# Optimization experiments

Measured on AMD Instinct MI355X. Metric: run time of the kernel, lower is better.

## Reference

```python
import jax, jax.numpy as jnp
import numpy as np

B, L, D, H = 2, 2048, 1024, 16
HD = D // H  # head_dim = 64


def setup_inputs() -> dict:
    key = jax.random.key(0)
    ks = jax.random.split(key, 11)
    s = 1.0 / np.sqrt(D)
    return {
        "query": jax.random.normal(ks[0], (B, L, D), jnp.float32),
        "key_": jax.random.normal(ks[1], (B, L, D), jnp.float32),
        "value": jax.random.normal(ks[2], (B, L, D), jnp.float32),
        "Wq": jax.random.normal(ks[3], (D, D), jnp.float32) * s,
        "bq": jnp.zeros((D,), jnp.float32),
        "Wk": jax.random.normal(ks[4], (D, D), jnp.float32) * s,
        "bk": jnp.zeros((D,), jnp.float32),
        "Wv": jax.random.normal(ks[5], (D, D), jnp.float32) * s,
        "bv": jnp.zeros((D,), jnp.float32),
        "Wo": jax.random.normal(ks[6], (D, D), jnp.float32) * s,
        "bo": jnp.zeros((D,), jnp.float32),
    }


def reference(query, key_, value, Wq, bq, Wk, bk, Wv, bv, Wo, bo):
    # q/k/v projections -> [B, H, L, HD]
    q = (query @ Wq + bq).reshape(B, L, H, HD).transpose(0, 2, 1, 3)
    k = (key_ @ Wk + bk).reshape(B, L, H, HD).transpose(0, 2, 1, 3)
    v = (value @ Wv + bv).reshape(B, L, H, HD).transpose(0, 2, 1, 3)
    # full attention matrix [B, H, L, L], scaled by sqrt(head_dim)
    scores = jnp.einsum('bhqd,bhkd->bhqk', q, k) / jnp.sqrt(jnp.float32(HD))
    attn = jax.nn.softmax(scores, axis=-1)
    out = jnp.einsum('bhqk,bhkd->bhqd', attn, v)  # [B, H, L, HD]
    out = out.transpose(0, 2, 1, 3).reshape(B, L, D)
    return out @ Wo + bo
```

## Files before the change

kernel.cpp:

```cpp
#include <hip/hip_runtime.h>
#include <hip/hip_bf16.h>
#include <stdint.h>

#define BATCH   2
#define SEQ     2048
#define D_MODEL 1024
#define NHEADS  16
#define HEADDIM 64
#define M_ROWS  (BATCH * SEQ)
#define NSPLIT  2

typedef __attribute__((ext_vector_type(8))) short bf16x8;
typedef __attribute__((ext_vector_type(4))) float f32x4;
typedef __attribute__((ext_vector_type(16))) float f32x16;
typedef __attribute__((ext_vector_type(2))) unsigned uint2v;

typedef __attribute__((address_space(3))) void       lds_void;
typedef const __attribute__((address_space(1))) void glb_void;

#define GLD_LDS16(g, l) \
  __builtin_amdgcn_global_load_lds((glb_void*)(g), (lds_void*)(l), 16, 0, 0)

#if __has_builtin(__builtin_amdgcn_exp2f)
#define EXP2(x) __builtin_amdgcn_exp2f(x)
#else
#define EXP2(x) exp2f(x)
#endif

__device__ __forceinline__ unsigned short f2bf(float f) {
  union { float f; unsigned u; } v; v.f = f;
  unsigned r = v.u + 0x7fff + ((v.u >> 16) & 1);
  return (unsigned short)(r >> 16);
}

__device__ __forceinline__ float bf2f(unsigned short u) {
  union { unsigned u; float f; } v; v.u = ((unsigned)u) << 16; return v.f;
}

__device__ __forceinline__ unsigned pkbf(float a, float b) {
  __hip_bfloat162 h = __float22bfloat162_rn(float2{a, b});
  union { __hip_bfloat162 h; unsigned u; } cv; cv.h = h; return cv.u;
}

__device__ __forceinline__ void plane32_swap(unsigned& a, unsigned& b) {
#if __has_builtin(__builtin_amdgcn_permlane32_swap)
  uint2v r = __builtin_amdgcn_permlane32_swap(a, b, false, false);
  a = r[0]; b = r[1];
#else
  asm volatile("s_nop 1\n\tv_permlane32_swap_b32 %0, %1\n\ts_nop 1"
               : "+v"(a), "+v"(b));
#endif
}

struct Cvt3Args { const float* x[3]; unsigned short* y[3]; };
__global__ void cvt_bf16_3(Cvt3Args a, int n) {
  const float* x = a.x[blockIdx.z];
  unsigned short* y = a.y[blockIdx.z];
  int i = (blockIdx.x * blockDim.x + threadIdx.x) * 4;
  if (i + 3 < n) {
    float4 v = *(const float4*)(x + i);
    ushort4 o; o.x = f2bf(v.x); o.y = f2bf(v.y); o.z = f2bf(v.z); o.w = f2bf(v.w);
    *(ushort4*)(y + i) = o;
  }
}

struct Wt4Args { const float* W[4]; unsigned short* WT[4]; };
__global__ void wtrans4(Wt4Args a) {
  const float* W = a.W[blockIdx.z];
  unsigned short* WT = a.WT[blockIdx.z];
  __shared__ float t[32][33];
  int bx = blockIdx.x * 32, by = blockIdx.y * 32;
  int tx = threadIdx.x, ty = threadIdx.y;
  t[ty][tx] = W[(size_t)(by + ty) * D_MODEL + bx + tx];
  __syncthreads();
  WT[(size_t)(bx + ty) * D_MODEL + by + tx] = f2bf(t[tx][ty]);
}

struct GemmArgs {
  const unsigned short* A[3];
  const unsigned short* B[3];
  const float*          bias[3];
  void*                 dst[3];
  int                   mode0;
};

__global__ __launch_bounds__(512, 2) void gemm_bf16(GemmArgs ga) {
  const int L = blockIdx.x;
  const int xcd = L & 7, slot = L >> 3;
  const int cb   = slot & 7;
  const int rest = slot >> 3;
  const int pp   = rest & 3;
  const int z    = rest >> 2;
  const int panel = pp * 8 + xcd;
  const int bn0 = cb * 128, bm0 = panel * 128;

  const unsigned short* __restrict__ A  = ga.A[z];
  const unsigned short* __restrict__ BT = ga.B[z];
  const float* __restrict__ bias        = ga.bias[z];
  void* dst = ga.dst[z];
  const int mode = ga.mode0 + z;

  const int K = D_MODEL;
  __shared__ unsigned short lds_a[128 * 64];
  __shared__ unsigned short lds_b[128 * 64];
  const int tid = threadIdx.x, wave = tid >> 6, lane = tid & 63;
  const int wr = wave >> 2, wc = wave & 3;
  const int lr = lane & 15, lq = lane >> 4;
  const int r8 = lane >> 3;
  const int sc = (lane & 7) ^ r8;

  f32x4 acc[4][2] = {};

  for (int k0 = 0; k0 < K; k0 += 64) {
    __syncthreads();
#pragma unroll
    for (int it = 0; it < 2; ++it) {
      int row = it * 64 + wave * 8 + r8;
      GLD_LDS16(A  + (size_t)(bm0 + row) * K + k0 + sc * 8,
                lds_a + (it * 512 + wave * 64) * 8);
      GLD_LDS16(BT + (size_t)(bn0 + row) * K + k0 + sc * 8,
                lds_b + (it * 512 + wave * 64) * 8);
    }
    __syncthreads();

#pragma unroll
    for (int kk = 0; kk < 2; ++kk) {
      bf16x8 af[4], bfr[2];
#pragma unroll
      for (int i = 0; i < 4; ++i) {
        const int ra = wr * 64 + i * 16 + lr;
        af[i] = *(const bf16x8*)(lds_a + ra * 64 + (((kk * 4 + lq) ^ (lr & 7)) * 8));
      }
#pragma unroll
      for (int j = 0; j < 2; ++j) {
        const int rb = wc * 32 + j * 16 + lr;
        bfr[j] = *(const bf16x8*)(lds_b + rb * 64 + (((kk * 4 + lq) ^ (lr & 7)) * 8));
      }
#pragma unroll
      for (int mi = 0; mi < 4; ++mi)
#pragma unroll
        for (int ni = 0; ni < 2; ++ni)
          acc[mi][ni] = __builtin_amdgcn_mfma_f32_16x16x32_bf16(af[mi], bfr[ni], acc[mi][ni], 0, 0, 0);
    }
  }

#pragma unroll
  for (int mi = 0; mi < 4; ++mi) {
#pragma unroll
    for (int ni = 0; ni < 2; ++ni) {
      const int n  = bn0 + wc * 32 + ni * 16 + lr;
      const float bv = bias[n];
      const int mb = bm0 + wr * 64 + mi * 16 + lq * 4;
      f32x4 v = acc[mi][ni];
      if (mode == 3) {
        float* o = (float*)dst;
#pragma unroll
        for (int r = 0; r < 4; ++r) o[(size_t)(mb + r) * D_MODEL + n] = v[r] + bv;
      } else if (mode == 2) {
        const int b = mb >> 11, l = mb & 2047;
        const int h = n >> 6, hd = n & 63;
        ushort4 pk;
        pk.x = f2bf(v[0] + bv); pk.y = f2bf(v[1] + bv);
        pk.z = f2bf(v[2] + bv); pk.w = f2bf(v[3] + bv);
        *(ushort4*)((unsigned short*)dst + ((size_t)((b * NHEADS + h) * HEADDIM + hd)) * SEQ + l) = pk;
      } else {
        unsigned short* o = (unsigned short*)dst;
        const int h = n >> 6, hd = n & 63;
#pragma unroll
        for (int r = 0; r < 4; ++r) {
          int m = mb + r; int b = m >> 11, l = m & 2047;
          o[((size_t)(b * NHEADS + h) * SEQ + l) * HEADDIM + hd] = f2bf(v[r] + bv);
        }
      }
    }
  }
}

__global__ __launch_bounds__(512, 4) void flash_attn(
    const unsigned short* __restrict__ Q,
    const unsigned short* __restrict__ Kb,
    const unsigned short* __restrict__ VT,
    unsigned short* __restrict__ Opart,
    float* __restrict__ lsum) {
  const int L = blockIdx.x;
  const int xcd = L & 7, slot = L >> 3;
  const int head = xcd * 4 + (slot >> 4);
  const int split = (slot >> 3) & 1;
  const int qb   = slot & 7;
  const int b = head >> 4, h = head & 15;
  const int kbase = split * (SEQ / NSPLIT);

  const int tid = threadIdx.x, wave = tid >> 6, lane = tid & 63;
  const int l31 = lane & 31, hi = lane >> 5;
  const int q0 = qb * 256 + wave * 32;

  const unsigned short* Qh = Q  + (size_t)head * SEQ * HEADDIM;
  const unsigned short* Kh = Kb + (size_t)head * SEQ * HEADDIM;
  const unsigned short* Vh = VT + (size_t)head * HEADDIM * SEQ;

  __shared__ unsigned short ldsK[2][64 * 64];
  __shared__ unsigned short ldsV[2][64 * 64];

  const int r8 = lane >> 3;
  const int sc = (lane & 7) ^ r8;
#define STAGE_KV(buf, k0_)                                                          \
  {                                                                                 \
    int row = wave * 8 + r8;                                                        \
    GLD_LDS16(Kh + (size_t)(k0_ + row) * HEADDIM + sc * 8,                          \
              &ldsK[buf][wave * 512]);                                              \
    GLD_LDS16(Vh + (size_t)row * SEQ + (k0_) + sc * 8,                              \
              &ldsV[buf][wave * 512]);                                              \
  }

  bf16x8 qf[4];
#pragma unroll
  for (int ds = 0; ds < 4; ++ds)
    qf[ds] = *(const bf16x8*)(Qh + (size_t)(q0 + l31) * HEADDIM + ds * 16 + hi * 8);

  f32x16 oacc[2] = {};
  float lpA = 0.f, lpB = 0.f;
  const float C  = 0.18033688011112f;
  const float nm = -C * 8.0f;

  STAGE_KV(0, kbase);
  __syncthreads();
  int cur = 0;

  const int NT = SEQ / NSPLIT / 64;
  for (int t = 0; t < NT; ++t) {
    if (t + 1 < NT) STAGE_KV(cur ^ 1, kbase + (t + 1) * 64);

    const unsigned short* lk = ldsK[cur];
    const unsigned short* lv = ldsV[cur];

    unsigned u[2][8];
#pragma unroll
    for (int kt = 0; kt < 2; ++kt) {
      const int row = kt * 32 + l31;
      const int swz = row & 7;
      f32x16 s = {};
      __builtin_amdgcn_s_setprio(1);
#pragma unroll
      for (int ds = 0; ds < 4; ++ds) {
        bf16x8 kf = *(const bf16x8*)(lk + row * 64 + (((ds * 2 + hi) ^ swz) * 8));
        s = __builtin_amdgcn_mfma_f32_32x32x16_bf16(kf, qf[ds], s, 0, 0, 0);
      }
      __builtin_amdgcn_s_setprio(0);
#pragma unroll
      for (int m = 0; m < 8; ++m) {
        float p0 = EXP2(fmaf(s[2 * m],     C, nm));
        float p1 = EXP2(fmaf(s[2 * m + 1], C, nm));
        lpA += p0; lpB += p1;
        u[kt][m] = pkbf(p0, p1);
      }
    }

    __builtin_amdgcn_s_setprio(1);
#pragma unroll
    for (int ks = 0; ks < 4; ++ks) {
      const int kt = ks >> 1, a = 4 * (ks & 1);
      unsigned c0 = u[kt][a],     c2 = u[kt][a + 2];
      unsigned c1 = u[kt][a + 1], c3 = u[kt][a + 3];
      plane32_swap(c0, c2);
      plane32_swap(c1, c3);
      union { unsigned w[4]; bf16x8 v; } pf;
      pf.w[0] = c0; pf.w[1] = c1; pf.w[2] = c2; pf.w[3] = c3;
#pragma unroll
      for (int dt = 0; dt < 2; ++dt) {
        const int row = dt * 32 + l31;
        bf16x8 vf = *(const bf16x8*)(lv + row * 64 + (((ks * 2 + hi) ^ (row & 7)) * 8));
        oacc[dt] = __builtin_amdgcn_mfma_f32_32x32x16_bf16(pf.v, vf, oacc[dt], 0, 0, 0);
      }
    }
    __builtin_amdgcn_s_setprio(0);

    __syncthreads();
    cur ^= 1;
  }

  float lpart = lpA + lpB;
  lpart += __shfl_xor(lpart, 32);
  float iv = 1.f / lpart;
  unsigned short* Opw = Opart + (size_t)split * M_ROWS * D_MODEL;
#pragma unroll
  for (int reg = 0; reg < 16; ++reg) {
    int qrow = (reg & 3) + 8 * (reg >> 2) + 4 * hi;
    float ivr = __shfl(iv, qrow);
    int qi = q0 + qrow;
#pragma unroll
    for (int dt = 0; dt < 2; ++dt)
      Opw[((size_t)(b * SEQ + qi) * NHEADS + h) * HEADDIM + dt * 32 + l31] =
          f2bf(oacc[dt][reg] * ivr);
  }
  if (hi == 0)
    lsum[((size_t)split * 32 + head) * SEQ + q0 + l31] = lpart;
#undef STAGE_KV
}

__global__ void combine2(const unsigned short* __restrict__ Op,
                         const float* __restrict__ lsum,
                         unsigned short* __restrict__ Obuf) {
  size_t i8 = ((size_t)blockIdx.x * blockDim.x + threadIdx.x) * 8;
  int row = (int)(i8 >> 10), col = (int)(i8 & 1023);
  int b = row >> 11, q = row & 2047;
  int head = b * NHEADS + (col >> 6);
  float l1 = lsum[(size_t)head * SEQ + q];
  float l2 = lsum[(size_t)(32 + head) * SEQ + q];
  float inv = 1.f / (l1 + l2);
  float w1 = l1 * inv, w2 = l2 * inv;
  bf16x8 a = *(const bf16x8*)(Op + i8);
  bf16x8 c = *(const bf16x8*)(Op + (size_t)M_ROWS * D_MODEL + i8);
  union { unsigned short u[8]; bf16x8 v; } o;
#pragma unroll
  for (int j = 0; j < 8; ++j)
    o.u[j] = f2bf(w1 * bf2f((unsigned short)a[j]) + w2 * bf2f((unsigned short)c[j]));
  *(bf16x8*)(Obuf + i8) = o.v;
}

extern "C" void kernel_launch(void* const* d_in, const int* in_sizes, int n_in,
                              void* d_out, int out_size, void* d_ws, size_t ws_size,
                              hipStream_t stream) {
  const float* query = (const float*)d_in[0];
  const float* key_  = (const float*)d_in[1];
  const float* value = (const float*)d_in[2];
  const float* Wq = (const float*)d_in[3];
  const float* bq = (const float*)d_in[4];
  const float* Wk = (const float*)d_in[5];
  const float* bk = (const float*)d_in[6];
  const float* Wv = (const float*)d_in[7];
  const float* bv = (const float*)d_in[8];
  const float* Wo = (const float*)d_in[9];
  const float* bo = (const float*)d_in[10];

  const size_t NX = (size_t)M_ROWS * D_MODEL;
  const size_t NW = (size_t)D_MODEL * D_MODEL;

  char* ws = (char*)d_ws;
  size_t off = 0;
  auto alloc = [&](size_t bytes) { char* p = ws + off; off += (bytes + 255) & ~255ULL; return p; };
  unsigned short* Xq    = (unsigned short*)alloc(NX * 2);
  unsigned short* Xk    = (unsigned short*)alloc(NX * 2);
  unsigned short* Xv    = (unsigned short*)alloc(NX * 2);
  unsigned short* WqT   = (unsigned short*)alloc(NW * 2);
  unsigned short* WkT   = (unsigned short*)alloc(NW * 2);
  unsigned short* WvT   = (unsigned short*)alloc(NW * 2);
  unsigned short* WoT   = (unsigned short*)alloc(NW * 2);
  unsigned short* Qh    = (unsigned short*)alloc(NX * 2);
  unsigned short* Kh    = (unsigned short*)alloc(NX * 2);
  unsigned short* VTh   = (unsigned short*)alloc(NX * 2);
  unsigned short* Obuf  = (unsigned short*)alloc(NX * 2);
  unsigned short* Opart = (unsigned short*)alloc(NSPLIT * NX * 2);
  float*          lbuf  = (float*)alloc(NSPLIT * 32 * SEQ * sizeof(float));

  Cvt3Args ca;
  ca.x[0] = query; ca.x[1] = key_; ca.x[2] = value;
  ca.y[0] = Xq;    ca.y[1] = Xk;   ca.y[2] = Xv;
  cvt_bf16_3<<<dim3((unsigned)(NX / 4 / 256), 1, 3), 256, 0, stream>>>(ca, (int)NX);

  Wt4Args wa;
  wa.W[0] = Wq; wa.W[1] = Wk; wa.W[2] = Wv; wa.W[3] = Wo;
  wa.WT[0] = WqT; wa.WT[1] = WkT; wa.WT[2] = WvT; wa.WT[3] = WoT;
  wtrans4<<<dim3(32, 32, 4), dim3(32, 32), 0, stream>>>(wa);

  GemmArgs pa = {};
  pa.A[0] = Xq;  pa.A[1] = Xk;  pa.A[2] = Xv;
  pa.B[0] = WqT; pa.B[1] = WkT; pa.B[2] = WvT;
  pa.bias[0] = bq; pa.bias[1] = bk; pa.bias[2] = bv;
  pa.dst[0] = Qh; pa.dst[1] = Kh; pa.dst[2] = VTh;
  pa.mode0 = 0;
  gemm_bf16<<<768, 512, 0, stream>>>(pa);

  flash_attn<<<512, 512, 0, stream>>>(Qh, Kh, VTh, Opart, lbuf);

  combine2<<<(unsigned)(NX / 8 / 256), 256, 0, stream>>>(Opart, lbuf, Obuf);

  GemmArgs fa = {};
  fa.A[0] = Obuf; fa.B[0] = WoT; fa.bias[0] = bo; fa.dst[0] = d_out; fa.mode0 = 3;
  gemm_bf16<<<256, 512, 0, stream>>>(fa);
}
```

Measured before the change: 134.0 us.

## Double-buffer LDS tiles in bf16 GEMM and raise priority around MFMA

The GEMM main loop now uses two LDS buffers, so the global-to-LDS load of the next K tile is issued before the MFMA work on the current tile. This cuts one barrier per iteration and overlaps memory latency with compute. It also wraps the MFMA block in s_setprio to favour math issue. LDS use per block doubles to 64KB, which may limit occupancy at 2 blocks per CU.

```diff
diff --git a/kernel.cpp b/kernel.cpp
--- a/kernel.cpp
+++ b/kernel.cpp
@@ -101,48 +101,64 @@
   const int mode = ga.mode0 + z;
 
   const int K = D_MODEL;
-  __shared__ unsigned short lds_a[128 * 64];
-  __shared__ unsigned short lds_b[128 * 64];
+  __shared__ unsigned short lds_a[2][128 * 64];
+  __shared__ unsigned short lds_b[2][128 * 64];
   const int tid = threadIdx.x, wave = tid >> 6, lane = tid & 63;
   const int wr = wave >> 2, wc = wave & 3;
   const int lr = lane & 15, lq = lane >> 4;
   const int r8 = lane >> 3;
   const int sc = (lane & 7) ^ r8;
 
+#define STAGE_AB(buf, k0_)                                                        \
+  {                                                                               \
+    _Pragma("unroll")                                                             \
+    for (int it = 0; it < 2; ++it) {                                              \
+      int row = it * 64 + wave * 8 + r8;                                          \
+      GLD_LDS16(A  + (size_t)(bm0 + row) * K + (k0_) + sc * 8,                    \
+                &lds_a[buf][(it * 512 + wave * 64) * 8]);                         \
+      GLD_LDS16(BT + (size_t)(bn0 + row) * K + (k0_) + sc * 8,                    \
+                &lds_b[buf][(it * 512 + wave * 64) * 8]);                         \
+    }                                                                             \
+  }
+
   f32x4 acc[4][2] = {};
 
-  for (int k0 = 0; k0 < K; k0 += 64) {
-    __syncthreads();
-#pragma unroll
-    for (int it = 0; it < 2; ++it) {
-      int row = it * 64 + wave * 8 + r8;
-      GLD_LDS16(A  + (size_t)(bm0 + row) * K + k0 + sc * 8,
-                lds_a + (it * 512 + wave * 64) * 8);
-      GLD_LDS16(BT + (size_t)(bn0 + row) * K + k0 + sc * 8,
-                lds_b + (it * 512 + wave * 64) * 8);
-    }
-    __syncthreads();
-
+  STAGE_AB(0, 0);
+  __syncthreads();
+  int cur = 0;
+
+  const int NT = K / 64;
+  for (int t = 0; t < NT; ++t) {
+    if (t + 1 < NT) STAGE_AB(cur ^ 1, (t + 1) * 64);
+
+    const unsigned short* la = lds_a[cur];
+    const unsigned short* lb = lds_b[cur];
 #pragma unroll
     for (int kk = 0; kk < 2; ++kk) {
       bf16x8 af[4], bfr[2];
 #pragma unroll
       for (int i = 0; i < 4; ++i) {
         const int ra = wr * 64 + i * 16 + lr;
-        af[i] = *(const bf16x8*)(lds_a + ra * 64 + (((kk * 4 + lq) ^ (lr & 7)) * 8));
+        af[i] = *(const bf16x8*)(la + ra * 64 + (((kk * 4 + lq) ^ (lr & 7)) * 8));
       }
 #pragma unroll
       for (int j = 0; j < 2; ++j) {
         const int rb = wc * 32 + j * 16 + lr;
-        bfr[j] = *(const bf16x8*)(lds_b + rb * 64 + (((kk * 4 + lq) ^ (lr & 7)) * 8));
-      }
+        bfr[j] = *(const bf16x8*)(lb + rb * 64 + (((kk * 4 + lq) ^ (lr & 7)) * 8));
+      }
+      __builtin_amdgcn_s_setprio(1);
 #pragma unroll
       for (int mi = 0; mi < 4; ++mi)
 #pragma unroll
         for (int ni = 0; ni < 2; ++ni)
           acc[mi][ni] = __builtin_amdgcn_mfma_f32_16x16x32_bf16(af[mi], bfr[ni], acc[mi][ni], 0, 0, 0);
+      __builtin_amdgcn_s_setprio(0);
     }
-  }
+
+    __syncthreads();
+    cur ^= 1;
+  }
+#undef STAGE_AB
 
 #pragma unroll
   for (int mi = 0; mi < 4; ++mi) {
```

After: 130.8 us. -2.4%, faster.
